# Kernel optimization log

Measured on AMD Instinct MI355X. Metric: run time of the kernel, lower is better.

## Reference

```python
import jax, jax.numpy as jnp
import numpy as np

U, I, D = 100000, 50000, 64
ALPHA = 0.2  # tf.nn.leaky_relu default


def seg_softmax(v, seg, n):
    # sparse row-wise softmax (tf.sparse.softmax equivalent)
    m = jax.ops.segment_max(v, seg, num_segments=n)
    e = jnp.exp(v - m[seg])
    s = jax.ops.segment_sum(e, seg, num_segments=n)
    return e / (s[seg] + 1e-12)


def spmm(att, row, col, x, n):
    # sparse_dense_matmul: out[r] = sum_e att[e] * x[col[e]]
    return jax.ops.segment_sum(att[:, None] * x[col], row, num_segments=n)


def edge_logit(raw, w, b):
    # Dense(1, sigmoid) on per-edge scalar, then exp (pre sparse-softmax)
    return jnp.exp(jax.nn.sigmoid(raw * w + b))


def graph_att(x, W, b1, w2, b2):
    # Dense(1, tanh) -> Dense(1, leaky_relu) on concat embeddings [N, 2D]
    h = jnp.tanh(x @ W + b1)  # [N]
    return jax.nn.leaky_relu(h * w2 + b2, ALPHA)


def setup_inputs() -> dict:
    key = jax.random.key(0)
    ks = jax.random.split(key, 24)
    Es, Eui, Eiu, B = 800000, 1000000, 1000000, 4096
    f32 = jnp.float32
    inp = {
        'user_embedding': jax.random.normal(ks[0], (U, D), f32) * 0.01,
        'item_embedding': jax.random.normal(ks[1], (I, D), f32) * 0.01,
        'snii1': jax.random.normal(ks[2], (Es,), f32),
        'snii2': jax.random.normal(ks[3], (Es,), f32),
        'ciii1': jax.random.normal(ks[4], (Eui,), f32),
        'ciii2': jax.random.normal(ks[5], (Eui,), f32),
        'icii1': jax.random.normal(ks[6], (Eiu,), f32),
        'icii2': jax.random.normal(ks[7], (Eiu,), f32) * 0.01,
        'low_att_w': jax.random.normal(ks[8], (6,), f32),
        'low_att_b': jax.random.normal(ks[9], (6,), f32),
        'att1_W': jax.random.normal(ks[10], (8, 2 * D), f32) * 0.1,
        'att1_b': jax.random.normal(ks[11], (8,), f32) * 0.1,
        'att2_w': jax.random.normal(ks[12], (8,), f32),
        'att2_b': jax.random.normal(ks[13], (8,), f32) * 0.1,
        'sn_row': jax.random.randint(ks[14], (Es,), 0, U, jnp.int32),
        'sn_col': jax.random.randint(ks[15], (Es,), 0, U, jnp.int32),
        'ci_row': jax.random.randint(ks[16], (Eui,), 0, U, jnp.int32),
        'ci_col': jax.random.randint(ks[17], (Eui,), 0, I, jnp.int32),
        'ic_row': jax.random.randint(ks[18], (Eiu,), 0, I, jnp.int32),
        'ic_col': jax.random.randint(ks[19], (Eiu,), 0, U, jnp.int32),
        'user_idx': jax.random.randint(ks[20], (B,), 0, U, jnp.int32),
        'item_idx': jax.random.randint(ks[21], (B,), 0, I, jnp.int32),
    }
    return inp


def reference(user_embedding, item_embedding, snii1, snii2, ciii1, ciii2,
              icii1, icii2, low_att_w, low_att_b, att1_W, att1_b, att2_w, att2_b,
              sn_row, sn_col, ci_row, ci_col, ic_row, ic_col, user_idx, item_idx):
    # low-level attention-weighted adjacency matrices (sparse softmax per row)
    sn1 = seg_softmax(edge_logit(snii1, low_att_w[0], low_att_b[0]), sn_row, U)
    sn2 = seg_softmax(edge_logit(snii2, low_att_w[1], low_att_b[1]), sn_row, U)
    ci1 = seg_softmax(edge_logit(ciii1, low_att_w[2], low_att_b[2]), ci_row, U)
    ci2 = seg_softmax(edge_logit(ciii2, low_att_w[3], low_att_b[3]), ci_row, U)
    ic1 = seg_softmax(edge_logit(icii1, low_att_w[4], low_att_b[4]), ic_row, I)
    ic2 = seg_softmax(edge_logit(icii2, low_att_w[5], low_att_b[5]), ic_row, I)

    u0, i0 = user_embedding, item_embedding

    def user_layer(u, it, att_sn, att_ci, k):
        u_from_i = spmm(att_ci, ci_row, ci_col, it, U)
        u_from_u = spmm(att_sn, sn_row, sn_col, u, U)
        a_int = jnp.exp(graph_att(jnp.concatenate([u, u_from_i], 1), att1_W[k], att1_b[k], att2_w[k], att2_b[k])) + 0.7
        a_soc = jnp.exp(graph_att(jnp.concatenate([u, u_from_u], 1), att1_W[k + 1], att1_b[k + 1], att2_w[k + 1], att2_b[k + 1])) + 0.3
        s = a_int + a_soc
        return 0.5 * u + 0.5 * ((a_int / s)[:, None] * u_from_i + (a_soc / s)[:, None] * u_from_u)

    def item_layer(u, it, att_ic, k):
        i_from_u = spmm(att_ic, ic_row, ic_col, u, I)
        a_self = jnp.exp(graph_att(jnp.concatenate([it, it], 1), att1_W[k], att1_b[k], att2_w[k], att2_b[k])) + 1.0
        a_cust = jnp.exp(graph_att(jnp.concatenate([it, i_from_u], 1), att1_W[k + 1], att1_b[k + 1], att2_w[k + 1], att2_b[k + 1])) + 1.0
        s = a_self + a_cust
        return (a_self / s)[:, None] * it + (a_cust / s)[:, None] * i_from_u

    u1 = user_layer(u0, i0, sn1, ci1, 0)
    i1 = item_layer(u0, i0, ic1, 4)
    u2 = user_layer(u1, i1, sn2, ci2, 2)
    i2 = item_layer(u1, i1, ic2, 6)

    fu = jnp.concatenate([u0, u1, u2], 1)  # [U, 3D]
    fi = jnp.concatenate([i0, i1, i2], 1)  # [I, 3D]
    return jax.nn.sigmoid(jnp.sum(fu[user_idx] * fi[item_idx], axis=1))  # [B]
```

## Files before the change

kernel.cpp:

```cpp
#include <hip/hip_runtime.h>
#include <math.h>

#define DIM 64
#define NBLK 512
#define NTHR 1024
#define KMAX 4096

typedef unsigned short ushort_t;
typedef unsigned int uint_t;
typedef unsigned char uchar_t;
typedef float v2f __attribute__((ext_vector_type(2)));

__device__ __forceinline__ ushort_t f2bf(float f) {
    uint_t u = __float_as_uint(f);
    return (ushort_t)((u + 0x7fffu + ((u >> 16) & 1u)) >> 16);
}


__global__ void count_cvt_kernel(const float* __restrict__ u0, const float* __restrict__ i0,
                                 uchar_t* __restrict__ ub, uchar_t* __restrict__ ib,
                                 size_t n8u, size_t n8t,
                                 const int* __restrict__ sn_row, const int* __restrict__ ci_row,
                                 const int* __restrict__ ic_row, int* __restrict__ cntBlk,
                                 int Es, int Eui, int Eiu, int U, int K) {
    __shared__ int h[KMAX];
    int b = blockIdx.x, tid = threadIdx.x;
    size_t gtid = (size_t)b * NTHR + tid;
    const size_t GT = (size_t)NBLK * NTHR;

    for (size_t i = gtid; i < n8t; i += GT) {
        const float4* src; uchar_t* dst; size_t di;
        if (i < n8u) { src = (const float4*)u0; dst = ub; di = i; }
        else         { src = (const float4*)i0; dst = ib; di = i - n8u; }
        float4 a = src[2 * di], c = src[2 * di + 1];
        int lo = 0, hi = 0;
        lo = __builtin_amdgcn_cvt_pk_fp8_f32(a.x * 256.0f, a.y * 256.0f, lo, false);
        lo = __builtin_amdgcn_cvt_pk_fp8_f32(a.z * 256.0f, a.w * 256.0f, lo, true);
        hi = __builtin_amdgcn_cvt_pk_fp8_f32(c.x * 256.0f, c.y * 256.0f, hi, false);
        hi = __builtin_amdgcn_cvt_pk_fp8_f32(c.z * 256.0f, c.w * 256.0f, hi, true);
        ((uint2*)dst)[di] = make_uint2((uint_t)lo, (uint_t)hi);
    }

    int E = Es + Eui + Eiu;
    int per = (E + NBLK - 1) / NBLK;
    int e0 = b * per, e1 = min(e0 + per, E);
    for (int i = tid; i < K; i += NTHR) h[i] = 0;
    __syncthreads();
    for (int e = e0 + tid; e < e1; e += NTHR) {
        int r;
        if (e < Es) r = sn_row[e];
        else if (e < Es + Eui) r = U + ci_row[e - Es];
        else r = 2 * U + ic_row[e - Es - Eui];
        atomicAdd(&h[r >> 6], 1);
    }
    __syncthreads();
    for (int i = tid; i < K; i += NTHR) cntBlk[(size_t)b * K + i] = h[i];
}


__global__ void base_kernel(const int* __restrict__ cntBlk, int* __restrict__ baseBlk,
                            int* __restrict__ total, int K) {
    int k = blockIdx.x * blockDim.x + threadIdx.x;
    if (k >= K) return;
    int s = 0;
    #pragma unroll 8
    for (int b = 0; b < NBLK; b++) {
        baseBlk[(size_t)b * K + k] = s;
        s += cntBlk[(size_t)b * K + k];
    }
    total[k] = s;
}


__global__ void scan_kernel(const int* __restrict__ total, int* __restrict__ bucketPtr,
                            int K, int E) {
    __shared__ int sums[NTHR];
    int tid = threadIdx.x;
    const int CH = KMAX / NTHR;
    int loc[CH];
    int base0 = tid * CH, s = 0;
    #pragma unroll
    for (int j = 0; j < CH; j++) {
        int idx = base0 + j;
        int v = (idx < K) ? total[idx] : 0;
        loc[j] = s; s += v;
    }
    sums[tid] = s;
    __syncthreads();
    for (int off = 1; off < NTHR; off <<= 1) {
        int t = 0;
        if (tid >= off) t = sums[tid - off];
        __syncthreads();
        if (tid >= off) sums[tid] += t;
        __syncthreads();
    }
    int offs = (tid > 0) ? sums[tid - 1] : 0;
    #pragma unroll
    for (int j = 0; j < CH; j++) {
        int idx = base0 + j;
        if (idx < K) bucketPtr[idx] = offs + loc[j];
    }
    if (tid == 0) bucketPtr[K] = E;
}


__global__ void place_kernel(const int* __restrict__ sn_row, const int* __restrict__ sn_col,
                             const int* __restrict__ ci_row, const int* __restrict__ ci_col,
                             const int* __restrict__ ic_row, const int* __restrict__ ic_col,
                             const float* __restrict__ snii1, const float* __restrict__ snii2,
                             const float* __restrict__ ciii1, const float* __restrict__ ciii2,
                             const float* __restrict__ icii1, const float* __restrict__ icii2,
                             const float* __restrict__ lw, const float* __restrict__ lb,
                             const int* __restrict__ bucketPtr, const int* __restrict__ baseBlk,
                             uint2* __restrict__ barr,
                             int Es, int Eui, int Eiu, int U, int K) {
    __shared__ int cur[KMAX];
    int E = Es + Eui + Eiu;
    int per = (E + NBLK - 1) / NBLK;
    int b = blockIdx.x;
    int e0 = b * per, e1 = min(e0 + per, E);
    for (int i = threadIdx.x; i < K; i += NTHR)
        cur[i] = bucketPtr[i] + baseBlk[(size_t)b * K + i];
    __syncthreads();
    for (int e = e0 + threadIdx.x; e < e1; e += NTHR) {
        int r, c, j1, j2;
        float r1, r2;
        if (e < Es) {
            r = sn_row[e]; c = sn_col[e]; r1 = snii1[e]; r2 = snii2[e]; j1 = 0; j2 = 1;
        } else if (e < Es + Eui) {
            int t = e - Es;
            r = U + ci_row[t]; c = ci_col[t]; r1 = ciii1[t]; r2 = ciii2[t]; j1 = 2; j2 = 3;
        } else {
            int t = e - Es - Eui;
            r = 2 * U + ic_row[t]; c = ic_col[t]; r1 = icii1[t]; r2 = icii2[t]; j1 = 4; j2 = 5;
        }
        float t1 = expf(expf(1.0f / (1.0f + expf(-(r1 * lw[j1] + lb[j1])))));
        float t2 = expf(expf(1.0f / (1.0f + expf(-(r2 * lw[j2] + lb[j2])))));
        uint_t packed = (uint_t)f2bf(t1) | ((uint_t)f2bf(t2) << 16);
        int k = r >> 6;
        int pos = atomicAdd(&cur[k], 1);
        barr[pos] = make_uint2(((uint_t)(r & 63) << 26) | (uint_t)c, packed);
    }
}


__global__ void finalize_kernel(const uint2* __restrict__ barr, const int* __restrict__ bucketPtr,
                                int* __restrict__ ptr, uint2* __restrict__ rec,
                                int R, int K, int E) {
    __shared__ int h[64], sc[64], cur2[64];
    int k = blockIdx.x;
    int s0 = bucketPtr[k], s1 = bucketPtr[k + 1];
    if (threadIdx.x < 64) { h[threadIdx.x] = 0; cur2[threadIdx.x] = 0; }
    __syncthreads();
    for (int e = s0 + threadIdx.x; e < s1; e += blockDim.x)
        atomicAdd(&h[(int)(barr[e].x >> 26)], 1);
    __syncthreads();
    if (threadIdx.x == 0) {
        int s = 0;
        #pragma unroll
        for (int i = 0; i < 64; i++) { sc[i] = s; s += h[i]; }
    }
    __syncthreads();
    if (threadIdx.x < 64) {
        int r = k * 64 + threadIdx.x;
        if (r < R) ptr[r] = s0 + sc[threadIdx.x];
    }
    if (k == K - 1 && threadIdx.x == 0) ptr[R] = E;
    __syncthreads();
    for (int e = s0 + threadIdx.x; e < s1; e += blockDim.x) {
        uint2 q = barr[e];
        int r6 = (int)(q.x >> 26);
        int rank = atomicAdd(&cur2[r6], 1);
        rec[s0 + sc[r6] + rank] = make_uint2(q.x & 0x3ffffffu, q.y);
    }
}


__device__ __forceinline__ float att_scalar(float dot, float b1, float w2, float b2, float addc) {
    float h = tanhf(dot + b1);
    float z = h * w2 + b2;
    float lr = z > 0.0f ? z : 0.2f * z;
    return expf(lr) + addc;
}

__device__ __forceinline__ void fp8_fma8v(v2f acc[4], uint2 v, float a) {
    v2f av = {a, a};
    acc[0] += av * __builtin_amdgcn_cvt_pk_f32_fp8((int)v.x, false);
    acc[1] += av * __builtin_amdgcn_cvt_pk_f32_fp8((int)v.x, true);
    acc[2] += av * __builtin_amdgcn_cvt_pk_f32_fp8((int)v.y, false);
    acc[3] += av * __builtin_amdgcn_cvt_pk_f32_fp8((int)v.y, true);
}

__device__ __forceinline__ float dot8_lanes(float d) {
    #pragma unroll
    for (int off = 1; off < 8; off <<= 1) d += __shfl_xor(d, off, 64);
    return d;
}

__device__ __forceinline__ void agg_row8(const uint2* __restrict__ rec, const uchar_t* __restrict__ tab,
                                         int e0, int e1, int l8, int lanebase,
                                         v2f acc[4], float& s) {
    if (e0 >= e1) return;
    int last = e1 - 1;
    int idx0 = e0 + l8;
    uint2 t0 = rec[min(idx0, last)];
    uint2 q;
    q.x = (idx0 <= last) ? t0.x : 0u;
    q.y = (idx0 <= last) ? t0.y : 0u;
    for (int base = e0; base < e1; base += 8) {
        int nidx = base + 8 + l8;
        uint2 tn = rec[min(nidx, last)];
        uint2 qn;
        qn.x = (nidx <= last) ? tn.x : 0u;
        qn.y = (nidx <= last) ? tn.y : 0u;
        s += __uint_as_float(q.y << 16);
        #pragma unroll
        for (int j = 0; j < 8; j++) {
            uint_t cx = __shfl(q.x, lanebase + j, 64);
            uint_t wy = __shfl(q.y, lanebase + j, 64);
            float a = __uint_as_float(wy << 16);
            uint2 v = ((const uint2*)(tab + (size_t)cx * DIM))[l8];
            fp8_fma8v(acc, v, a);
        }
        q = qn;
    }
}

__global__ void layer1_kernel(const uchar_t* __restrict__ ub8, const uchar_t* __restrict__ ib8,
                              const float* __restrict__ u0, const float* __restrict__ i0,
                              const int* __restrict__ ptr, const uint2* __restrict__ rec,
                              const float* __restrict__ W1, const float* __restrict__ b1v,
                              const float* __restrict__ w2v, const float* __restrict__ b2v,
                              float* __restrict__ u1, float* __restrict__ i1, int U, int I) {
    int gid = blockIdx.x * (blockDim.x >> 3) + (threadIdx.x >> 3);
    int lane = threadIdx.x & 63;
    int l8 = lane & 7;
    int lanebase = lane & 56;
    if (gid >= U + I) return;
    bool is_user = gid < U;
    int r = is_user ? gid : gid - U;

    v2f A[4]  = {{0.f, 0.f}, {0.f, 0.f}, {0.f, 0.f}, {0.f, 0.f}};
    v2f Bv[4] = {{0.f, 0.f}, {0.f, 0.f}, {0.f, 0.f}, {0.f, 0.f}};
    float s_a = 0.f, s_b = 0.f;

    if (is_user) {
        agg_row8(rec, ib8, ptr[U + r], ptr[U + r + 1], l8, lanebase, A, s_a);
        agg_row8(rec, ub8, ptr[r], ptr[r + 1], l8, lanebase, Bv, s_b);
    } else {
        agg_row8(rec, ub8, ptr[2 * U + r], ptr[2 * U + r + 1], l8, lanebase, A, s_a);
    }
    s_a = dot8_lanes(s_a);
    s_b = dot8_lanes(s_b);

    float ka = (1.0f / (s_a + 1e-12f)) * 0.00390625f;
    float kb = (1.0f / (s_b + 1e-12f)) * 0.00390625f;
    float ac[8], bc[8];
    #pragma unroll
    for (int j = 0; j < 4; j++) {
        ac[2 * j] = A[j][0] * ka;  ac[2 * j + 1] = A[j][1] * ka;
        bc[2 * j] = Bv[j][0] * kb; bc[2 * j + 1] = Bv[j][1] * kb;
    }

    const float* selfp = (is_user ? u0 : i0) + (size_t)r * DIM + 8 * l8;
    float4 s0 = *(const float4*)selfp;
    float4 s1 = *(const float4*)(selfp + 4);
    float sf[8] = {s0.x, s0.y, s0.z, s0.w, s1.x, s1.y, s1.z, s1.w};
    int k = is_user ? 0 : 4;
    const float* Wa = W1 + k * 2 * DIM;
    const float* Wb = Wa + 2 * DIM;
    float d1 = 0.f, d2 = 0.f;
    #pragma unroll
    for (int j = 0; j < 8; j++) {
        float wa0 = Wa[8 * l8 + j], wa1 = Wa[DIM + 8 * l8 + j];
        float wb0 = Wb[8 * l8 + j], wb1 = Wb[DIM + 8 * l8 + j];
        if (is_user) {
            d1 += sf[j] * wa0 + ac[j] * wa1;
            d2 += sf[j] * wb0 + bc[j] * wb1;
        } else {
            d1 += sf[j] * (wa0 + wa1);
            d2 += sf[j] * wb0 + ac[j] * wb1;
        }
    }
    d1 = dot8_lanes(d1);
    d2 = dot8_lanes(d2);

    float out8[8];
    float* op;
    if (is_user) {
        float a_int = att_scalar(d1, b1v[0], w2v[0], b2v[0], 0.7f);
        float a_soc = att_scalar(d2, b1v[1], w2v[1], b2v[1], 0.3f);
        float sg = a_int + a_soc;
        float wi = a_int / sg, ws = a_soc / sg;
        #pragma unroll
        for (int j = 0; j < 8; j++)
            out8[j] = 0.5f * sf[j] + 0.5f * (wi * ac[j] + ws * bc[j]);
        op = u1 + (size_t)r * DIM + 8 * l8;
    } else {
        float a_self = att_scalar(d1, b1v[4], w2v[4], b2v[4], 1.0f);
        float a_cust = att_scalar(d2, b1v[5], w2v[5], b2v[5], 1.0f);
        float sg = a_self + a_cust;
        float wi = a_self / sg, ws = a_cust / sg;
        #pragma unroll
        for (int j = 0; j < 8; j++)
            out8[j] = wi * sf[j] + ws * ac[j];
        op = i1 + (size_t)r * DIM + 8 * l8;
    }
    *(float4*)op = make_float4(out8[0], out8[1], out8[2], out8[3]);
    *(float4*)(op + 4) = make_float4(out8[4], out8[5], out8[6], out8[7]);
}

__global__ void layer2_kernel(const float* __restrict__ u1, const float* __restrict__ i1,
                              const int* __restrict__ ptr, const uint2* __restrict__ rec,
                              const float* __restrict__ W1, const float* __restrict__ b1v,
                              const float* __restrict__ w2v, const float* __restrict__ b2v,
                              const int* __restrict__ uidx, const int* __restrict__ iidx,
                              float* __restrict__ u2s, float* __restrict__ i2s, int U, int B) {
    int wid = blockIdx.x * (blockDim.x >> 6) + (threadIdx.x >> 6);
    int lane = threadIdx.x & 63;
    if (wid >= 2 * B) return;
    int g = lane >> 3, l8 = lane & 7;
    bool is_user = wid < B;
    int b = is_user ? wid : wid - B;
    int r = is_user ? uidx[b] : iidx[b];

    float acc_a[8] = {0, 0, 0, 0, 0, 0, 0, 0};
    float acc_b[8] = {0, 0, 0, 0, 0, 0, 0, 0};
    float s_a = 0.f, s_b = 0.f;

    if (is_user) {
        int e0 = ptr[U + r], e1 = ptr[U + r + 1];
        for (int e = e0 + g; e < e1; e += 8) {
            uint2 q = rec[e];
            float a = __uint_as_float(q.y & 0xffff0000u);
            s_a += a;
            const float4* rp = (const float4*)(i1 + (size_t)q.x * DIM);
            float4 v0 = rp[2 * l8], v1 = rp[2 * l8 + 1];
            acc_a[0] = fmaf(a, v0.x, acc_a[0]); acc_a[1] = fmaf(a, v0.y, acc_a[1]);
            acc_a[2] = fmaf(a, v0.z, acc_a[2]); acc_a[3] = fmaf(a, v0.w, acc_a[3]);
            acc_a[4] = fmaf(a, v1.x, acc_a[4]); acc_a[5] = fmaf(a, v1.y, acc_a[5]);
            acc_a[6] = fmaf(a, v1.z, acc_a[6]); acc_a[7] = fmaf(a, v1.w, acc_a[7]);
        }
        e0 = ptr[r]; e1 = ptr[r + 1];
        for (int e = e0 + g; e < e1; e += 8) {
            uint2 q = rec[e];
            float a = __uint_as_float(q.y & 0xffff0000u);
            s_b += a;
            const float4* rp = (const float4*)(u1 + (size_t)q.x * DIM);
            float4 v0 = rp[2 * l8], v1 = rp[2 * l8 + 1];
            acc_b[0] = fmaf(a, v0.x, acc_b[0]); acc_b[1] = fmaf(a, v0.y, acc_b[1]);
            acc_b[2] = fmaf(a, v0.z, acc_b[2]); acc_b[3] = fmaf(a, v0.w, acc_b[3]);
            acc_b[4] = fmaf(a, v1.x, acc_b[4]); acc_b[5] = fmaf(a, v1.y, acc_b[5]);
            acc_b[6] = fmaf(a, v1.z, acc_b[6]); acc_b[7] = fmaf(a, v1.w, acc_b[7]);
        }
    } else {
        int e0 = ptr[2 * U + r], e1 = ptr[2 * U + r + 1];
        for (int e = e0 + g; e < e1; e += 8) {
            uint2 q = rec[e];
            float a = __uint_as_float(q.y & 0xffff0000u);
            s_a += a;
            const float4* rp = (const float4*)(u1 + (size_t)q.x * DIM);
            float4 v0 = rp[2 * l8], v1 = rp[2 * l8 + 1];
            acc_a[0] = fmaf(a, v0.x, acc_a[0]); acc_a[1] = fmaf(a, v0.y, acc_a[1]);
            acc_a[2] = fmaf(a, v0.z, acc_a[2]); acc_a[3] = fmaf(a, v0.w, acc_a[3]);
            acc_a[4] = fmaf(a, v1.x, acc_a[4]); acc_a[5] = fmaf(a, v1.y, acc_a[5]);
            acc_a[6] = fmaf(a, v1.z, acc_a[6]); acc_a[7] = fmaf(a, v1.w, acc_a[7]);
        }
    }

    #pragma unroll
    for (int off = 8; off < 64; off <<= 1) {
        s_a += __shfl_xor(s_a, off, 64);
        #pragma unroll
        for (int j = 0; j < 8; j++) acc_a[j] += __shfl_xor(acc_a[j], off, 64);
    }
    if (is_user) {
        #pragma unroll
        for (int off = 8; off < 64; off <<= 1) {
            s_b += __shfl_xor(s_b, off, 64);
            #pragma unroll
            for (int j = 0; j < 8; j++) acc_b[j] += __shfl_xor(acc_b[j], off, 64);
        }
    }
    float ka = 1.0f / (s_a + 1e-12f);
    float kb = 1.0f / (s_b + 1e-12f);

    if (g == 0) {
        #pragma unroll
        for (int j = 0; j < 8; j++) { acc_a[j] *= ka; acc_b[j] *= kb; }
        const float* selfp = (is_user ? u1 : i1) + (size_t)r * DIM + 8 * l8;
        float4 s0 = *(const float4*)selfp;
        float4 s1 = *(const float4*)(selfp + 4);
        float sf[8] = {s0.x, s0.y, s0.z, s0.w, s1.x, s1.y, s1.z, s1.w};
        int k = is_user ? 2 : 6;
        const float* Wa = W1 + k * 2 * DIM;
        const float* Wb = Wa + 2 * DIM;
        float d1 = 0.f, d2 = 0.f;
        #pragma unroll
        for (int j = 0; j < 8; j++) {
            float wa0 = Wa[8 * l8 + j], wa1 = Wa[DIM + 8 * l8 + j];
            float wb0 = Wb[8 * l8 + j], wb1 = Wb[DIM + 8 * l8 + j];
            if (is_user) {
                d1 += sf[j] * wa0 + acc_a[j] * wa1;
                d2 += sf[j] * wb0 + acc_b[j] * wb1;
            } else {
                d1 += sf[j] * (wa0 + wa1);
                d2 += sf[j] * wb0 + acc_a[j] * wb1;
            }
        }
        d1 = dot8_lanes(d1);
        d2 = dot8_lanes(d2);

        float out8[8];
        float* op;
        if (is_user) {
            float a_int = att_scalar(d1, b1v[2], w2v[2], b2v[2], 0.7f);
            float a_soc = att_scalar(d2, b1v[3], w2v[3], b2v[3], 0.3f);
            float sg = a_int + a_soc;
            float wi = a_int / sg, ws = a_soc / sg;
            #pragma unroll
            for (int j = 0; j < 8; j++)
                out8[j] = 0.5f * sf[j] + 0.5f * (wi * acc_a[j] + ws * acc_b[j]);
            op = u2s + (size_t)b * DIM + 8 * l8;
        } else {
            float a_self = att_scalar(d1, b1v[6], w2v[6], b2v[6], 1.0f);
            float a_cust = att_scalar(d2, b1v[7], w2v[7], b2v[7], 1.0f);
            float sg = a_self + a_cust;
            float wi = a_self / sg, ws = a_cust / sg;
            #pragma unroll
            for (int j = 0; j < 8; j++)
                out8[j] = wi * sf[j] + ws * acc_a[j];
            op = i2s + (size_t)b * DIM + 8 * l8;
        }
        *(float4*)op = make_float4(out8[0], out8[1], out8[2], out8[3]);
        *(float4*)(op + 4) = make_float4(out8[4], out8[5], out8[6], out8[7]);
    }
}


__global__ void final_kernel(const float* __restrict__ u0, const float* __restrict__ u1,
                             const float* __restrict__ u2s,
                             const float* __restrict__ i0, const float* __restrict__ i1,
                             const float* __restrict__ i2s,
                             const int* __restrict__ uidx, const int* __restrict__ iidx,
                             float* __restrict__ out, int n) {
    int b = blockIdx.x * (blockDim.x >> 6) + (threadIdx.x >> 6);
    int lane = threadIdx.x & 63;
    if (b >= n) return;
    size_t ur = (size_t)uidx[b] * DIM + lane;
    size_t ir = (size_t)iidx[b] * DIM + lane;
    size_t sr = (size_t)b * DIM + lane;
    float acc = u0[ur] * i0[ir] + u1[ur] * i1[ir] + u2s[sr] * i2s[sr];
    #pragma unroll
    for (int off = 32; off > 0; off >>= 1) acc += __shfl_xor(acc, off, 64);
    if (lane == 0) out[b] = 1.0f / (1.0f + expf(-acc));
}


extern "C" void kernel_launch(void* const* d_in, const int* in_sizes, int n_in,
                              void* d_out, int out_size, void* d_ws, size_t ws_size,
                              hipStream_t stream) {
    const float* user_emb = (const float*)d_in[0];
    const float* item_emb = (const float*)d_in[1];
    const float* snii1 = (const float*)d_in[2];
    const float* snii2 = (const float*)d_in[3];
    const float* ciii1 = (const float*)d_in[4];
    const float* ciii2 = (const float*)d_in[5];
    const float* icii1 = (const float*)d_in[6];
    const float* icii2 = (const float*)d_in[7];
    const float* low_w = (const float*)d_in[8];
    const float* low_b = (const float*)d_in[9];
    const float* att1_W = (const float*)d_in[10];
    const float* att1_b = (const float*)d_in[11];
    const float* att2_w = (const float*)d_in[12];
    const float* att2_b = (const float*)d_in[13];
    const int* sn_row = (const int*)d_in[14];
    const int* sn_col = (const int*)d_in[15];
    const int* ci_row = (const int*)d_in[16];
    const int* ci_col = (const int*)d_in[17];
    const int* ic_row = (const int*)d_in[18];
    const int* ic_col = (const int*)d_in[19];
    const int* user_idx = (const int*)d_in[20];
    const int* item_idx = (const int*)d_in[21];
    float* out = (float*)d_out;

    const int Es  = in_sizes[2];
    const int Eui = in_sizes[4];
    const int Eiu = in_sizes[6];
    const int U = in_sizes[0] / DIM;
    const int I = in_sizes[1] / DIM;
    const int B = in_sizes[20];
    const int R = 2 * U + I;
    const int E = Es + Eui + Eiu;
    const int K = (R + 63) >> 6;

    char* wsb = (char*)d_ws;
    size_t off = 0;
    auto alloc = [&](size_t n_units) {
        off = (off + 3) & ~(size_t)3;
        void* p = wsb + off * 4; off += n_units; return p;
    };

    int* cntBlk    = (int*)alloc((size_t)NBLK * K);
    int* baseBlk   = (int*)alloc((size_t)NBLK * K);
    int* total     = (int*)alloc(K);
    int* bucketPtr = (int*)alloc(K + 1);
    int* ptr       = (int*)alloc(R + 1);
    uint2* barr    = (uint2*)alloc((size_t)E * 2);
    uint2* rec     = (uint2*)alloc((size_t)E * 2);
    uchar_t* ub8 = (uchar_t*)alloc((size_t)U * DIM / 4);
    uchar_t* ib8 = (uchar_t*)alloc((size_t)I * DIM / 4);
    float* u1  = (float*)alloc((size_t)U * DIM);
    float* i1  = (float*)alloc((size_t)I * DIM);
    float* u2s = (float*)alloc((size_t)B * DIM);
    float* i2s = (float*)alloc((size_t)B * DIM);
    (void)ws_size;

    size_t n8u = (size_t)U * DIM / 8, n8t = (size_t)(U + I) * DIM / 8;

    count_cvt_kernel<<<NBLK, NTHR, 0, stream>>>(user_emb, item_emb, ub8, ib8, n8u, n8t,
                                                sn_row, ci_row, ic_row, cntBlk,
                                                Es, Eui, Eiu, U, K);
    base_kernel<<<(K + 255) / 256, 256, 0, stream>>>(cntBlk, baseBlk, total, K);
    scan_kernel<<<1, NTHR, 0, stream>>>(total, bucketPtr, K, E);
    place_kernel<<<NBLK, NTHR, 0, stream>>>(sn_row, sn_col, ci_row, ci_col, ic_row, ic_col,
                                            snii1, snii2, ciii1, ciii2, icii1, icii2,
                                            low_w, low_b, bucketPtr, baseBlk, barr,
                                            Es, Eui, Eiu, U, K);
    finalize_kernel<<<K, 256, 0, stream>>>(barr, bucketPtr, ptr, rec, R, K, E);

    layer1_kernel<<<(U + I + 31) / 32, 256, 0, stream>>>(ub8, ib8, user_emb, item_emb,
        ptr, rec, att1_W, att1_b, att2_w, att2_b, u1, i1, U, I);

    layer2_kernel<<<(2 * B + 3) / 4, 256, 0, stream>>>(u1, i1, ptr, rec,
        att1_W, att1_b, att2_w, att2_b, user_idx, item_idx, u2s, i2s, U, B);

    final_kernel<<<(B + 3) / 4, 256, 0, stream>>>(user_emb, u1, u2s, item_emb, i1, i2s,
                                                  user_idx, item_idx, out, B);
}
```

Before: 344.4 us.

## Replace two-level bucket sort CSR build with per-row atomic counting sort

Replaces the block-histogram, per-block base and two-pass bucket placement with a direct per-row degree count using global atomics, a two-kernel chunked exclusive scan, and a single placement pass that writes edges straight into CSR order through per-row global atomic cursors. This removes the large per-block count/base arrays, the intermediate bucket array and the finalize kernel. In exchange it relies on global atomics spread over 250K rows, and edge order within a row becomes nondeterministic. The bsum reduction covers only 64 chunks, which is enough for R up to 262144.

```diff
diff --git a/kernel.cpp b/kernel.cpp
--- a/kernel.cpp
+++ b/kernel.cpp
@@ -4,7 +4,7 @@
 #define DIM 64
 #define NBLK 512
 #define NTHR 1024
-#define KMAX 4096
+#define SCH  4096
 
 typedef unsigned short ushort_t;
 typedef unsigned int uint_t;
@@ -21,11 +21,9 @@
                                  uchar_t* __restrict__ ub, uchar_t* __restrict__ ib,
                                  size_t n8u, size_t n8t,
                                  const int* __restrict__ sn_row, const int* __restrict__ ci_row,
-                                 const int* __restrict__ ic_row, int* __restrict__ cntBlk,
-                                 int Es, int Eui, int Eiu, int U, int K) {
-    __shared__ int h[KMAX];
-    int b = blockIdx.x, tid = threadIdx.x;
-    size_t gtid = (size_t)b * NTHR + tid;
+                                 const int* __restrict__ ic_row, int* __restrict__ deg,
+                                 int Es, int Eui, int Eiu, int U) {
+    size_t gtid = (size_t)blockIdx.x * NTHR + threadIdx.x;
     const size_t GT = (size_t)NBLK * NTHR;
 
     for (size_t i = gtid; i < n8t; i += GT) {
@@ -42,47 +40,27 @@
     }
 
     int E = Es + Eui + Eiu;
-    int per = (E + NBLK - 1) / NBLK;
-    int e0 = b * per, e1 = min(e0 + per, E);
-    for (int i = tid; i < K; i += NTHR) h[i] = 0;
-    __syncthreads();
-    for (int e = e0 + tid; e < e1; e += NTHR) {
+    for (size_t e = gtid; e < (size_t)E; e += GT) {
         int r;
-        if (e < Es) r = sn_row[e];
-        else if (e < Es + Eui) r = U + ci_row[e - Es];
+        if (e < (size_t)Es) r = sn_row[e];
+        else if (e < (size_t)(Es + Eui)) r = U + ci_row[e - Es];
         else r = 2 * U + ic_row[e - Es - Eui];
-        atomicAdd(&h[r >> 6], 1);
-    }
-    __syncthreads();
-    for (int i = tid; i < K; i += NTHR) cntBlk[(size_t)b * K + i] = h[i];
-}
-
-
-__global__ void base_kernel(const int* __restrict__ cntBlk, int* __restrict__ baseBlk,
-                            int* __restrict__ total, int K) {
-    int k = blockIdx.x * blockDim.x + threadIdx.x;
-    if (k >= K) return;
+        atomicAdd(&deg[r], 1);
+    }
+}
+
+
+__global__ void scan1_kernel(const int* __restrict__ deg, int* __restrict__ tmp,
+                             int* __restrict__ bsum, int R) {
+    __shared__ int sums[NTHR];
+    int tid = threadIdx.x, b = blockIdx.x;
+    int base0 = b * SCH + tid * 4;
+    int loc[4];
     int s = 0;
-    #pragma unroll 8
-    for (int b = 0; b < NBLK; b++) {
-        baseBlk[(size_t)b * K + k] = s;
-        s += cntBlk[(size_t)b * K + k];
-    }
-    total[k] = s;
-}
-
-
-__global__ void scan_kernel(const int* __restrict__ total, int* __restrict__ bucketPtr,
-                            int K, int E) {
-    __shared__ int sums[NTHR];
-    int tid = threadIdx.x;
-    const int CH = KMAX / NTHR;
-    int loc[CH];
-    int base0 = tid * CH, s = 0;
-    #pragma unroll
-    for (int j = 0; j < CH; j++) {
+    #pragma unroll
+    for (int j = 0; j < 4; j++) {
         int idx = base0 + j;
-        int v = (idx < K) ? total[idx] : 0;
+        int v = (idx < R) ? deg[idx] : 0;
         loc[j] = s; s += v;
     }
     sums[tid] = s;
@@ -96,11 +74,38 @@
     }
     int offs = (tid > 0) ? sums[tid - 1] : 0;
     #pragma unroll
-    for (int j = 0; j < CH; j++) {
+    for (int j = 0; j < 4; j++) {
         int idx = base0 + j;
-        if (idx < K) bucketPtr[idx] = offs + loc[j];
-    }
-    if (tid == 0) bucketPtr[K] = E;
+        if (idx < R) tmp[idx] = offs + loc[j];
+    }
+    if (tid == NTHR - 1) bsum[b] = sums[NTHR - 1];
+}
+
+
+__global__ void ptr_kernel(const int* __restrict__ tmp, const int* __restrict__ bsum,
+                           int* __restrict__ ptr, int* __restrict__ cur,
+                           int R, int E) {
+    __shared__ int soff;
+    int b = blockIdx.x, tid = threadIdx.x;
+    if (tid < 64) {
+        int v = (tid < b) ? bsum[tid] : 0;
+        #pragma unroll
+        for (int o = 32; o > 0; o >>= 1) v += __shfl_xor(v, o, 64);
+        if (tid == 0) soff = v;
+    }
+    __syncthreads();
+    int off = soff;
+    int base0 = b * SCH + tid * 4;
+    #pragma unroll
+    for (int j = 0; j < 4; j++) {
+        int idx = base0 + j;
+        if (idx < R) {
+            int v = tmp[idx] + off;
+            ptr[idx] = v;
+            cur[idx] = v;
+        }
+    }
+    if (b == 0 && tid == 0) ptr[R] = E;
 }
 
 
@@ -111,67 +116,28 @@
                              const float* __restrict__ ciii1, const float* __restrict__ ciii2,
                              const float* __restrict__ icii1, const float* __restrict__ icii2,
                              const float* __restrict__ lw, const float* __restrict__ lb,
-                             const int* __restrict__ bucketPtr, const int* __restrict__ baseBlk,
-                             uint2* __restrict__ barr,
-                             int Es, int Eui, int Eiu, int U, int K) {
-    __shared__ int cur[KMAX];
+                             int* __restrict__ cur, uint2* __restrict__ rec,
+                             int Es, int Eui, int Eiu, int U) {
     int E = Es + Eui + Eiu;
-    int per = (E + NBLK - 1) / NBLK;
-    int b = blockIdx.x;
-    int e0 = b * per, e1 = min(e0 + per, E);
-    for (int i = threadIdx.x; i < K; i += NTHR)
-        cur[i] = bucketPtr[i] + baseBlk[(size_t)b * K + i];
-    __syncthreads();
-    for (int e = e0 + threadIdx.x; e < e1; e += NTHR) {
+    size_t gtid = (size_t)blockIdx.x * NTHR + threadIdx.x;
+    const size_t GT = (size_t)NBLK * NTHR;
+    for (size_t e = gtid; e < (size_t)E; e += GT) {
         int r, c, j1, j2;
         float r1, r2;
-        if (e < Es) {
+        if (e < (size_t)Es) {
             r = sn_row[e]; c = sn_col[e]; r1 = snii1[e]; r2 = snii2[e]; j1 = 0; j2 = 1;
-        } else if (e < Es + Eui) {
-            int t = e - Es;
+        } else if (e < (size_t)(Es + Eui)) {
+            size_t t = e - Es;
             r = U + ci_row[t]; c = ci_col[t]; r1 = ciii1[t]; r2 = ciii2[t]; j1 = 2; j2 = 3;
         } else {
-            int t = e - Es - Eui;
+            size_t t = e - Es - Eui;
             r = 2 * U + ic_row[t]; c = ic_col[t]; r1 = icii1[t]; r2 = icii2[t]; j1 = 4; j2 = 5;
         }
         float t1 = expf(expf(1.0f / (1.0f + expf(-(r1 * lw[j1] + lb[j1])))));
         float t2 = expf(expf(1.0f / (1.0f + expf(-(r2 * lw[j2] + lb[j2])))));
         uint_t packed = (uint_t)f2bf(t1) | ((uint_t)f2bf(t2) << 16);
-        int k = r >> 6;
-        int pos = atomicAdd(&cur[k], 1);
-        barr[pos] = make_uint2(((uint_t)(r & 63) << 26) | (uint_t)c, packed);
-    }
-}
-
-
-__global__ void finalize_kernel(const uint2* __restrict__ barr, const int* __restrict__ bucketPtr,
-                                int* __restrict__ ptr, uint2* __restrict__ rec,
-                                int R, int K, int E) {
-    __shared__ int h[64], sc[64], cur2[64];
-    int k = blockIdx.x;
-    int s0 = bucketPtr[k], s1 = bucketPtr[k + 1];
-    if (threadIdx.x < 64) { h[threadIdx.x] = 0; cur2[threadIdx.x] = 0; }
-    __syncthreads();
-    for (int e = s0 + threadIdx.x; e < s1; e += blockDim.x)
-        atomicAdd(&h[(int)(barr[e].x >> 26)], 1);
-    __syncthreads();
-    if (threadIdx.x == 0) {
-        int s = 0;
-        #pragma unroll
-        for (int i = 0; i < 64; i++) { sc[i] = s; s += h[i]; }
-    }
-    __syncthreads();
-    if (threadIdx.x < 64) {
-        int r = k * 64 + threadIdx.x;
-        if (r < R) ptr[r] = s0 + sc[threadIdx.x];
-    }
-    if (k == K - 1 && threadIdx.x == 0) ptr[R] = E;
-    __syncthreads();
-    for (int e = s0 + threadIdx.x; e < s1; e += blockDim.x) {
-        uint2 q = barr[e];
-        int r6 = (int)(q.x >> 26);
-        int rank = atomicAdd(&cur2[r6], 1);
-        rec[s0 + sc[r6] + rank] = make_uint2(q.x & 0x3ffffffu, q.y);
+        int pos = atomicAdd(&cur[r], 1);
+        rec[pos] = make_uint2((uint_t)c, packed);
     }
 }
 
@@ -492,7 +458,7 @@
     const int B = in_sizes[20];
     const int R = 2 * U + I;
     const int E = Es + Eui + Eiu;
-    const int K = (R + 63) >> 6;
+    const int NCH = (R + SCH - 1) / SCH;
 
     char* wsb = (char*)d_ws;
     size_t off = 0;
@@ -501,13 +467,12 @@
         void* p = wsb + off * 4; off += n_units; return p;
     };
 
-    int* cntBlk    = (int*)alloc((size_t)NBLK * K);
-    int* baseBlk   = (int*)alloc((size_t)NBLK * K);
-    int* total     = (int*)alloc(K);
-    int* bucketPtr = (int*)alloc(K + 1);
-    int* ptr       = (int*)alloc(R + 1);
-    uint2* barr    = (uint2*)alloc((size_t)E * 2);
-    uint2* rec     = (uint2*)alloc((size_t)E * 2);
+    int* deg  = (int*)alloc(R);
+    int* tmp  = (int*)alloc(R);
+    int* bsum = (int*)alloc(64);
+    int* ptr  = (int*)alloc(R + 1);
+    int* cur  = (int*)alloc(R);
+    uint2* rec = (uint2*)alloc((size_t)E * 2);
     uchar_t* ub8 = (uchar_t*)alloc((size_t)U * DIM / 4);
     uchar_t* ib8 = (uchar_t*)alloc((size_t)I * DIM / 4);
     float* u1  = (float*)alloc((size_t)U * DIM);
@@ -518,16 +483,16 @@
 
     size_t n8u = (size_t)U * DIM / 8, n8t = (size_t)(U + I) * DIM / 8;
 
+    hipMemsetAsync(deg, 0, sizeof(int) * (size_t)R, stream);
     count_cvt_kernel<<<NBLK, NTHR, 0, stream>>>(user_emb, item_emb, ub8, ib8, n8u, n8t,
-                                                sn_row, ci_row, ic_row, cntBlk,
-                                                Es, Eui, Eiu, U, K);
-    base_kernel<<<(K + 255) / 256, 256, 0, stream>>>(cntBlk, baseBlk, total, K);
-    scan_kernel<<<1, NTHR, 0, stream>>>(total, bucketPtr, K, E);
+                                                sn_row, ci_row, ic_row, deg,
+                                                Es, Eui, Eiu, U);
+    scan1_kernel<<<NCH, NTHR, 0, stream>>>(deg, tmp, bsum, R);
+    ptr_kernel<<<NCH, NTHR, 0, stream>>>(tmp, bsum, ptr, cur, R, E);
     place_kernel<<<NBLK, NTHR, 0, stream>>>(sn_row, sn_col, ci_row, ci_col, ic_row, ic_col,
                                             snii1, snii2, ciii1, ciii2, icii1, icii2,
-                                            low_w, low_b, bucketPtr, baseBlk, barr,
-                                            Es, Eui, Eiu, U, K);
-    finalize_kernel<<<K, 256, 0, stream>>>(barr, bucketPtr, ptr, rec, R, K, E);
+                                            low_w, low_b, cur, rec,
+                                            Es, Eui, Eiu, U);
 
     layer1_kernel<<<(U + I + 31) / 32, 256, 0, stream>>>(ub8, ib8, user_emb, item_emb,
         ptr, rec, att1_W, att1_b, att2_w, att2_b, u1, i1, U, I);
```

After: 499.7 us. +45.1%, slower.

## Shrink bucketing grid, move fp8 conversion into finalize, use wave scan

Applied to the files above, without the earlier changes.

Reduces the number of blocks used for edge counting and placement, which shrinks the per-block bucket histogram arrays and the serial base-offset loop. The fp8 embedding conversion moves from the count kernel into the finalize kernel's wide grid, and the single-thread 64-entry prefix sum becomes a wave shuffle scan. The trade-off is fewer blocks doing the exp-heavy placement work, which may leave many compute units idle.

```diff
diff --git a/kernel.cpp b/kernel.cpp
--- a/kernel.cpp
+++ b/kernel.cpp
@@ -2,9 +2,10 @@
 #include <math.h>
 
 #define DIM 64
-#define NBLK 512
+#define NBLK_P 64
 #define NTHR 1024
 #define KMAX 4096
+
 
 typedef unsigned short ushort_t;
 typedef unsigned int uint_t;
@@ -17,32 +18,13 @@
 }
 
 
-__global__ void count_cvt_kernel(const float* __restrict__ u0, const float* __restrict__ i0,
-                                 uchar_t* __restrict__ ub, uchar_t* __restrict__ ib,
-                                 size_t n8u, size_t n8t,
-                                 const int* __restrict__ sn_row, const int* __restrict__ ci_row,
-                                 const int* __restrict__ ic_row, int* __restrict__ cntBlk,
-                                 int Es, int Eui, int Eiu, int U, int K) {
+__global__ void count_kernel(const int* __restrict__ sn_row, const int* __restrict__ ci_row,
+                             const int* __restrict__ ic_row, int* __restrict__ cntBlk,
+                             int Es, int Eui, int Eiu, int U, int K) {
     __shared__ int h[KMAX];
     int b = blockIdx.x, tid = threadIdx.x;
-    size_t gtid = (size_t)b * NTHR + tid;
-    const size_t GT = (size_t)NBLK * NTHR;
-
-    for (size_t i = gtid; i < n8t; i += GT) {
-        const float4* src; uchar_t* dst; size_t di;
-        if (i < n8u) { src = (const float4*)u0; dst = ub; di = i; }
-        else         { src = (const float4*)i0; dst = ib; di = i - n8u; }
-        float4 a = src[2 * di], c = src[2 * di + 1];
-        int lo = 0, hi = 0;
-        lo = __builtin_amdgcn_cvt_pk_fp8_f32(a.x * 256.0f, a.y * 256.0f, lo, false);
-        lo = __builtin_amdgcn_cvt_pk_fp8_f32(a.z * 256.0f, a.w * 256.0f, lo, true);
-        hi = __builtin_amdgcn_cvt_pk_fp8_f32(c.x * 256.0f, c.y * 256.0f, hi, false);
-        hi = __builtin_amdgcn_cvt_pk_fp8_f32(c.z * 256.0f, c.w * 256.0f, hi, true);
-        ((uint2*)dst)[di] = make_uint2((uint_t)lo, (uint_t)hi);
-    }
-
     int E = Es + Eui + Eiu;
-    int per = (E + NBLK - 1) / NBLK;
+    int per = (E + NBLK_P - 1) / NBLK_P;
     int e0 = b * per, e1 = min(e0 + per, E);
     for (int i = tid; i < K; i += NTHR) h[i] = 0;
     __syncthreads();
@@ -64,7 +46,7 @@
     if (k >= K) return;
     int s = 0;
     #pragma unroll 8
-    for (int b = 0; b < NBLK; b++) {
+    for (int b = 0; b < NBLK_P; b++) {
         baseBlk[(size_t)b * K + k] = s;
         s += cntBlk[(size_t)b * K + k];
     }
@@ -116,7 +98,7 @@
                              int Es, int Eui, int Eiu, int U, int K) {
     __shared__ int cur[KMAX];
     int E = Es + Eui + Eiu;
-    int per = (E + NBLK - 1) / NBLK;
+    int per = (E + NBLK_P - 1) / NBLK_P;
     int b = blockIdx.x;
     int e0 = b * per, e1 = min(e0 + per, E);
     for (int i = threadIdx.x; i < K; i += NTHR)
@@ -144,30 +126,50 @@
 }
 
 
-__global__ void finalize_kernel(const uint2* __restrict__ barr, const int* __restrict__ bucketPtr,
+__global__ void finalize_kernel(const float* __restrict__ u0f, const float* __restrict__ i0f,
+                                uchar_t* __restrict__ ub, uchar_t* __restrict__ ib,
+                                size_t n8u, size_t n8t,
+                                const uint2* __restrict__ barr, const int* __restrict__ bucketPtr,
                                 int* __restrict__ ptr, uint2* __restrict__ rec,
                                 int R, int K, int E) {
+    size_t gt = (size_t)blockIdx.x * blockDim.x + threadIdx.x;
+    size_t GT = (size_t)gridDim.x * blockDim.x;
+    for (size_t i = gt; i < n8t; i += GT) {
+        const float4* src; uchar_t* dst; size_t di;
+        if (i < n8u) { src = (const float4*)u0f; dst = ub; di = i; }
+        else         { src = (const float4*)i0f; dst = ib; di = i - n8u; }
+        float4 a = src[2 * di], c = src[2 * di + 1];
+        int lo = 0, hi = 0;
+        lo = __builtin_amdgcn_cvt_pk_fp8_f32(a.x * 256.0f, a.y * 256.0f, lo, false);
+        lo = __builtin_amdgcn_cvt_pk_fp8_f32(a.z * 256.0f, a.w * 256.0f, lo, true);
+        hi = __builtin_amdgcn_cvt_pk_fp8_f32(c.x * 256.0f, c.y * 256.0f, hi, false);
+        hi = __builtin_amdgcn_cvt_pk_fp8_f32(c.z * 256.0f, c.w * 256.0f, hi, true);
+        ((uint2*)dst)[di] = make_uint2((uint_t)lo, (uint_t)hi);
+    }
+
     __shared__ int h[64], sc[64], cur2[64];
     int k = blockIdx.x;
     int s0 = bucketPtr[k], s1 = bucketPtr[k + 1];
     if (threadIdx.x < 64) { h[threadIdx.x] = 0; cur2[threadIdx.x] = 0; }
     __syncthreads();
-    for (int e = s0 + threadIdx.x; e < s1; e += blockDim.x)
+    for (int e = s0 + (int)threadIdx.x; e < s1; e += (int)blockDim.x)
         atomicAdd(&h[(int)(barr[e].x >> 26)], 1);
     __syncthreads();
-    if (threadIdx.x == 0) {
-        int s = 0;
-        #pragma unroll
-        for (int i = 0; i < 64; i++) { sc[i] = s; s += h[i]; }
-    }
-    __syncthreads();
     if (threadIdx.x < 64) {
-        int r = k * 64 + threadIdx.x;
-        if (r < R) ptr[r] = s0 + sc[threadIdx.x];
+        int v = h[threadIdx.x];
+        int inc = v;
+        #pragma unroll
+        for (int off = 1; off < 64; off <<= 1) {
+            int t = __shfl_up(inc, off, 64);
+            if ((int)threadIdx.x >= off) inc += t;
+        }
+        sc[threadIdx.x] = inc - v;
+        int r = k * 64 + (int)threadIdx.x;
+        if (r < R) ptr[r] = s0 + inc - v;
     }
     if (k == K - 1 && threadIdx.x == 0) ptr[R] = E;
     __syncthreads();
-    for (int e = s0 + threadIdx.x; e < s1; e += blockDim.x) {
+    for (int e = s0 + (int)threadIdx.x; e < s1; e += (int)blockDim.x) {
         uint2 q = barr[e];
         int r6 = (int)(q.x >> 26);
         int rank = atomicAdd(&cur2[r6], 1);
@@ -501,8 +503,8 @@
         void* p = wsb + off * 4; off += n_units; return p;
     };
 
-    int* cntBlk    = (int*)alloc((size_t)NBLK * K);
-    int* baseBlk   = (int*)alloc((size_t)NBLK * K);
+    int* cntBlk    = (int*)alloc((size_t)NBLK_P * K);
+    int* baseBlk   = (int*)alloc((size_t)NBLK_P * K);
     int* total     = (int*)alloc(K);
     int* bucketPtr = (int*)alloc(K + 1);
     int* ptr       = (int*)alloc(R + 1);
@@ -518,16 +520,16 @@
 
     size_t n8u = (size_t)U * DIM / 8, n8t = (size_t)(U + I) * DIM / 8;
 
-    count_cvt_kernel<<<NBLK, NTHR, 0, stream>>>(user_emb, item_emb, ub8, ib8, n8u, n8t,
-                                                sn_row, ci_row, ic_row, cntBlk,
-                                                Es, Eui, Eiu, U, K);
+    count_kernel<<<NBLK_P, NTHR, 0, stream>>>(sn_row, ci_row, ic_row, cntBlk,
+                                              Es, Eui, Eiu, U, K);
     base_kernel<<<(K + 255) / 256, 256, 0, stream>>>(cntBlk, baseBlk, total, K);
     scan_kernel<<<1, NTHR, 0, stream>>>(total, bucketPtr, K, E);
-    place_kernel<<<NBLK, NTHR, 0, stream>>>(sn_row, sn_col, ci_row, ci_col, ic_row, ic_col,
-                                            snii1, snii2, ciii1, ciii2, icii1, icii2,
-                                            low_w, low_b, bucketPtr, baseBlk, barr,
-                                            Es, Eui, Eiu, U, K);
-    finalize_kernel<<<K, 256, 0, stream>>>(barr, bucketPtr, ptr, rec, R, K, E);
+    place_kernel<<<NBLK_P, NTHR, 0, stream>>>(sn_row, sn_col, ci_row, ci_col, ic_row, ic_col,
+                                              snii1, snii2, ciii1, ciii2, icii1, icii2,
+                                              low_w, low_b, bucketPtr, baseBlk, barr,
+                                              Es, Eui, Eiu, U, K);
+    finalize_kernel<<<K, 256, 0, stream>>>(user_emb, item_emb, ub8, ib8, n8u, n8t,
+                                           barr, bucketPtr, ptr, rec, R, K, E);
 
     layer1_kernel<<<(U + I + 31) / 32, 256, 0, stream>>>(ub8, ib8, user_emb, item_emb,
         ptr, rec, att1_W, att1_b, att2_w, att2_b, u1, i1, U, I);
```

New measurement: 376.4 us. +9.3%, slower.

## Coarsen CSR build buckets from 64 to 1024 rows to shrink histograms and scans

Applied to the files above, without the earlier changes.

The two-level counting sort that builds CSR now uses coarse buckets of 1024 rows, about 245, instead of 64-row buckets, about 3900. Per-block histograms and offset arrays shrink roughly 16x, so the serial per-bucket base loop and the single-block scan become small wavefront-shuffle scans. Finalize then sorts within each 1024-row bucket using a 1024-entry LDS histogram and scan. The trade-off is fewer, larger finalize blocks, and column indices are now limited to 22 bits.

```diff
diff --git a/kernel.cpp b/kernel.cpp
--- a/kernel.cpp
+++ b/kernel.cpp
@@ -2,9 +2,11 @@
 #include <math.h>
 
 #define DIM 64
-#define NBLK 512
+#define NBLK_P 512
 #define NTHR 1024
-#define KMAX 4096
+#define CBSZ 1024
+#define CBMAX 256
+
 
 typedef unsigned short ushort_t;
 typedef unsigned int uint_t;
@@ -21,12 +23,12 @@
                                  uchar_t* __restrict__ ub, uchar_t* __restrict__ ib,
                                  size_t n8u, size_t n8t,
                                  const int* __restrict__ sn_row, const int* __restrict__ ci_row,
-                                 const int* __restrict__ ic_row, int* __restrict__ cntBlk,
-                                 int Es, int Eui, int Eiu, int U, int K) {
-    __shared__ int h[KMAX];
+                                 const int* __restrict__ ic_row, int* __restrict__ cnt,
+                                 int Es, int Eui, int Eiu, int U, int CB) {
+    __shared__ int h[CBMAX];
     int b = blockIdx.x, tid = threadIdx.x;
     size_t gtid = (size_t)b * NTHR + tid;
-    const size_t GT = (size_t)NBLK * NTHR;
+    const size_t GT = (size_t)NBLK_P * NTHR;
 
     for (size_t i = gtid; i < n8t; i += GT) {
         const float4* src; uchar_t* dst; size_t di;
@@ -42,65 +44,61 @@
     }
 
     int E = Es + Eui + Eiu;
-    int per = (E + NBLK - 1) / NBLK;
+    int per = (E + NBLK_P - 1) / NBLK_P;
     int e0 = b * per, e1 = min(e0 + per, E);
-    for (int i = tid; i < K; i += NTHR) h[i] = 0;
+    if (tid < CBMAX) h[tid] = 0;
     __syncthreads();
     for (int e = e0 + tid; e < e1; e += NTHR) {
         int r;
         if (e < Es) r = sn_row[e];
         else if (e < Es + Eui) r = U + ci_row[e - Es];
         else r = 2 * U + ic_row[e - Es - Eui];
-        atomicAdd(&h[r >> 6], 1);
-    }
-    __syncthreads();
-    for (int i = tid; i < K; i += NTHR) cntBlk[(size_t)b * K + i] = h[i];
-}
-
-
-__global__ void base_kernel(const int* __restrict__ cntBlk, int* __restrict__ baseBlk,
-                            int* __restrict__ total, int K) {
-    int k = blockIdx.x * blockDim.x + threadIdx.x;
-    if (k >= K) return;
-    int s = 0;
-    #pragma unroll 8
-    for (int b = 0; b < NBLK; b++) {
-        baseBlk[(size_t)b * K + k] = s;
-        s += cntBlk[(size_t)b * K + k];
-    }
-    total[k] = s;
-}
-
-
-__global__ void scan_kernel(const int* __restrict__ total, int* __restrict__ bucketPtr,
-                            int K, int E) {
-    __shared__ int sums[NTHR];
-    int tid = threadIdx.x;
-    const int CH = KMAX / NTHR;
-    int loc[CH];
-    int base0 = tid * CH, s = 0;
-    #pragma unroll
-    for (int j = 0; j < CH; j++) {
-        int idx = base0 + j;
-        int v = (idx < K) ? total[idx] : 0;
-        loc[j] = s; s += v;
-    }
-    sums[tid] = s;
-    __syncthreads();
-    for (int off = 1; off < NTHR; off <<= 1) {
-        int t = 0;
-        if (tid >= off) t = sums[tid - off];
-        __syncthreads();
-        if (tid >= off) sums[tid] += t;
-        __syncthreads();
-    }
-    int offs = (tid > 0) ? sums[tid - 1] : 0;
-    #pragma unroll
-    for (int j = 0; j < CH; j++) {
-        int idx = base0 + j;
-        if (idx < K) bucketPtr[idx] = offs + loc[j];
-    }
-    if (tid == 0) bucketPtr[K] = E;
+        atomicAdd(&h[r >> 10], 1);
+    }
+    __syncthreads();
+    if (tid < CB) cnt[(size_t)b * CB + tid] = h[tid];
+}
+
+
+__global__ void blkscan_kernel(const int* __restrict__ cnt, int* __restrict__ blkoff,
+                               int* __restrict__ total, int CB) {
+    int c = blockIdx.x;
+    int b = threadIdx.x;
+    int v = cnt[(size_t)b * CB + c];
+    int lane = b & 63, wid = b >> 6;
+    int inc = v;
+    #pragma unroll
+    for (int off = 1; off < 64; off <<= 1) {
+        int x = __shfl_up(inc, off, 64);
+        if (lane >= off) inc += x;
+    }
+    __shared__ int ws[NBLK_P / 64];
+    if (lane == 63) ws[wid] = inc;
+    __syncthreads();
+    int woff = 0;
+    for (int j = 0; j < wid; j++) woff += ws[j];
+    blkoff[(size_t)b * CB + c] = inc - v + woff;
+    if (b == NBLK_P - 1) total[c] = inc + woff;
+}
+
+
+__global__ void cstart_kernel(const int* __restrict__ total, int* __restrict__ cstart, int CB) {
+    int t = threadIdx.x;
+    int v = (t < CB) ? total[t] : 0;
+    int lane = t & 63, wid = t >> 6;
+    int inc = v;
+    #pragma unroll
+    for (int off = 1; off < 64; off <<= 1) {
+        int x = __shfl_up(inc, off, 64);
+        if (lane >= off) inc += x;
+    }
+    __shared__ int ws[4];
+    if (lane == 63) ws[wid] = inc;
+    __syncthreads();
+    int woff = 0;
+    for (int j = 0; j < wid; j++) woff += ws[j];
+    if (t < CB) cstart[t] = inc - v + woff;
+    if (t == CB - 1) cstart[CB] = inc + woff;
 }
 
 
@@ -111,18 +109,18 @@
                              const float* __restrict__ ciii1, const float* __restrict__ ciii2,
                              const float* __restrict__ icii1, const float* __restrict__ icii2,
                              const float* __restrict__ lw, const float* __restrict__ lb,
-                             const int* __restrict__ bucketPtr, const int* __restrict__ baseBlk,
+                             const int* __restrict__ cstart, const int* __restrict__ blkoff,
                              uint2* __restrict__ barr,
-                             int Es, int Eui, int Eiu, int U, int K) {
-    __shared__ int cur[KMAX];
+                             int Es, int Eui, int Eiu, int U, int CB) {
+    __shared__ int cur[CBMAX];
     int E = Es + Eui + Eiu;
-    int per = (E + NBLK - 1) / NBLK;
+    int per = (E + NBLK_P - 1) / NBLK_P;
     int b = blockIdx.x;
     int e0 = b * per, e1 = min(e0 + per, E);
-    for (int i = threadIdx.x; i < K; i += NTHR)
-        cur[i] = bucketPtr[i] + baseBlk[(size_t)b * K + i];
-    __syncthreads();
-    for (int e = e0 + threadIdx.x; e < e1; e += NTHR) {
+    if (threadIdx.x < CB)
+        cur[threadIdx.x] = cstart[threadIdx.x] + blkoff[(size_t)b * CB + threadIdx.x];
+    __syncthreads();
+    for (int e = e0 + (int)threadIdx.x; e < e1; e += NTHR) {
         int r, c, j1, j2;
         float r1, r2;
         if (e < Es) {
@@ -137,41 +135,49 @@
         float t1 = expf(expf(1.0f / (1.0f + expf(-(r1 * lw[j1] + lb[j1])))));
         float t2 = expf(expf(1.0f / (1.0f + expf(-(r2 * lw[j2] + lb[j2])))));
         uint_t packed = (uint_t)f2bf(t1) | ((uint_t)f2bf(t2) << 16);
-        int k = r >> 6;
-        int pos = atomicAdd(&cur[k], 1);
-        barr[pos] = make_uint2(((uint_t)(r & 63) << 26) | (uint_t)c, packed);
-    }
-}
-
-
-__global__ void finalize_kernel(const uint2* __restrict__ barr, const int* __restrict__ bucketPtr,
+        int cb = r >> 10;
+        int pos = atomicAdd(&cur[cb], 1);
+        barr[pos] = make_uint2(((uint_t)(r & 1023) << 22) | (uint_t)c, packed);
+    }
+}
+
+
+__global__ void finalize_kernel(const uint2* __restrict__ barr, const int* __restrict__ cstart,
                                 int* __restrict__ ptr, uint2* __restrict__ rec,
-                                int R, int K, int E) {
-    __shared__ int h[64], sc[64], cur2[64];
-    int k = blockIdx.x;
-    int s0 = bucketPtr[k], s1 = bucketPtr[k + 1];
-    if (threadIdx.x < 64) { h[threadIdx.x] = 0; cur2[threadIdx.x] = 0; }
-    __syncthreads();
-    for (int e = s0 + threadIdx.x; e < s1; e += blockDim.x)
-        atomicAdd(&h[(int)(barr[e].x >> 26)], 1);
-    __syncthreads();
-    if (threadIdx.x == 0) {
-        int s = 0;
-        #pragma unroll
-        for (int i = 0; i < 64; i++) { sc[i] = s; s += h[i]; }
-    }
-    __syncthreads();
-    if (threadIdx.x < 64) {
-        int r = k * 64 + threadIdx.x;
-        if (r < R) ptr[r] = s0 + sc[threadIdx.x];
-    }
-    if (k == K - 1 && threadIdx.x == 0) ptr[R] = E;
-    __syncthreads();
-    for (int e = s0 + threadIdx.x; e < s1; e += blockDim.x) {
+                                int R, int CB) {
+    __shared__ int hist[CBSZ];
+    __shared__ int cur2[CBSZ];
+    __shared__ int ws[NTHR / 64];
+    int c = blockIdx.x, tid = threadIdx.x;
+    int s0 = cstart[c], s1 = cstart[c + 1];
+    hist[tid] = 0;
+    __syncthreads();
+    for (int e = s0 + tid; e < s1; e += NTHR)
+        atomicAdd(&hist[barr[e].x >> 22], 1);
+    __syncthreads();
+    int v = hist[tid];
+    int lane = tid & 63, wid = tid >> 6;
+    int inc = v;
+    #pragma unroll
+    for (int off = 1; off < 64; off <<= 1) {
+        int x = __shfl_up(inc, off, 64);
+        if (lane >= off) inc += x;
+    }
+    if (lane == 63) ws[wid] = inc;
+    __syncthreads();
+    int woff = 0;
+    for (int j = 0; j < wid; j++) woff += ws[j];
+    int p0 = s0 + inc - v + woff;
+    int r = c * CBSZ + tid;
+    if (r < R) ptr[r] = p0;
+    cur2[tid] = p0;
+    if (c == CB - 1 && tid == 0) ptr[R] = cstart[CB];
+    __syncthreads();
+    for (int e = s0 + tid; e < s1; e += NTHR) {
         uint2 q = barr[e];
-        int r6 = (int)(q.x >> 26);
-        int rank = atomicAdd(&cur2[r6], 1);
-        rec[s0 + sc[r6] + rank] = make_uint2(q.x & 0x3ffffffu, q.y);
+        int rin = (int)(q.x >> 22);
+        int pos = atomicAdd(&cur2[rin], 1);
+        rec[pos] = make_uint2(q.x & 0x3FFFFFu, q.y);
     }
 }
 
@@ -492,7 +498,7 @@
     const int B = in_sizes[20];
     const int R = 2 * U + I;
     const int E = Es + Eui + Eiu;
-    const int K = (R + 63) >> 6;
+    const int CB = (R + CBSZ - 1) / CBSZ;
 
     char* wsb = (char*)d_ws;
     size_t off = 0;
@@ -501,13 +507,13 @@
         void* p = wsb + off * 4; off += n_units; return p;
     };
 
-    int* cntBlk    = (int*)alloc((size_t)NBLK * K);
-    int* baseBlk   = (int*)alloc((size_t)NBLK * K);
-    int* total     = (int*)alloc(K);
-    int* bucketPtr = (int*)alloc(K + 1);
-    int* ptr       = (int*)alloc(R + 1);
-    uint2* barr    = (uint2*)alloc((size_t)E * 2);
-    uint2* rec     = (uint2*)alloc((size_t)E * 2);
+    int* cnt    = (int*)alloc((size_t)NBLK_P * CB);
+    int* blkoff = (int*)alloc((size_t)NBLK_P * CB);
+    int* total  = (int*)alloc(CB);
+    int* cstart = (int*)alloc(CB + 1);
+    int* ptr    = (int*)alloc(R + 1);
+    uint2* barr = (uint2*)alloc((size_t)E * 2);
+    uint2* rec  = (uint2*)alloc((size_t)E * 2);
     uchar_t* ub8 = (uchar_t*)alloc((size_t)U * DIM / 4);
     uchar_t* ib8 = (uchar_t*)alloc((size_t)I * DIM / 4);
     float* u1  = (float*)alloc((size_t)U * DIM);
@@ -518,16 +524,16 @@
 
     size_t n8u = (size_t)U * DIM / 8, n8t = (size_t)(U + I) * DIM / 8;
 
-    count_cvt_kernel<<<NBLK, NTHR, 0, stream>>>(user_emb, item_emb, ub8, ib8, n8u, n8t,
-                                                sn_row, ci_row, ic_row, cntBlk,
-                                                Es, Eui, Eiu, U, K);
-    base_kernel<<<(K + 255) / 256, 256, 0, stream>>>(cntBlk, baseBlk, total, K);
-    scan_kernel<<<1, NTHR, 0, stream>>>(total, bucketPtr, K, E);
-    place_kernel<<<NBLK, NTHR, 0, stream>>>(sn_row, sn_col, ci_row, ci_col, ic_row, ic_col,
-                                            snii1, snii2, ciii1, ciii2, icii1, icii2,
-                                            low_w, low_b, bucketPtr, baseBlk, barr,
-                                            Es, Eui, Eiu, U, K);
-    finalize_kernel<<<K, 256, 0, stream>>>(barr, bucketPtr, ptr, rec, R, K, E);
+    count_cvt_kernel<<<NBLK_P, NTHR, 0, stream>>>(user_emb, item_emb, ub8, ib8, n8u, n8t,
+                                                  sn_row, ci_row, ic_row, cnt,
+                                                  Es, Eui, Eiu, U, CB);
+    blkscan_kernel<<<CB, NBLK_P, 0, stream>>>(cnt, blkoff, total, CB);
+    cstart_kernel<<<1, 256, 0, stream>>>(total, cstart, CB);
+    place_kernel<<<NBLK_P, NTHR, 0, stream>>>(sn_row, sn_col, ci_row, ci_col, ic_row, ic_col,
+                                              snii1, snii2, ciii1, ciii2, icii1, icii2,
+                                              low_w, low_b, cstart, blkoff, barr,
+                                              Es, Eui, Eiu, U, CB);
+    finalize_kernel<<<CB, NTHR, 0, stream>>>(barr, cstart, ptr, rec, R, CB);
 
     layer1_kernel<<<(U + I + 31) / 32, 256, 0, stream>>>(ub8, ib8, user_emb, item_emb,
         ptr, rec, att1_W, att1_b, att2_w, att2_b, u1, i1, U, I);
```

Result: faster. 305.6 us (-11.3%).
